# Kernel tuning notes

Measured on AMD Instinct MI355X. Metric: run time of the kernel, lower is better.

Reference implementation:

```python
import jax, jax.numpy as jnp
import numpy as np

N_NODES = 100000
N_EDGES = 1600000
IN_DIM = 64
HID_DIM = 64
NUM_CLASSES = 10
NUM_GRAPHS = 64


def setup_inputs() -> dict:
    key = jax.random.key(0)
    ks = jax.random.split(key, 8)
    x = jax.random.normal(ks[0], (N_NODES, IN_DIM), dtype=jnp.float32)
    edge_index = jax.random.randint(ks[1], (2, N_EDGES), 0, N_NODES, dtype=jnp.int32)
    batch = jnp.sort(jax.random.randint(ks[2], (N_NODES,), 0, NUM_GRAPHS, dtype=jnp.int32))
    # GCNConv weights (glorot-ish scale) and biases
    W1 = jax.random.normal(ks[3], (IN_DIM, HID_DIM), dtype=jnp.float32) / np.sqrt(IN_DIM)
    b1 = jnp.zeros((HID_DIM,), dtype=jnp.float32)
    W2 = jax.random.normal(ks[4], (HID_DIM, HID_DIM), dtype=jnp.float32) / np.sqrt(HID_DIM)
    b2 = jnp.zeros((HID_DIM,), dtype=jnp.float32)
    Wlin = jax.random.normal(ks[5], (HID_DIM, NUM_CLASSES), dtype=jnp.float32) / np.sqrt(HID_DIM)
    blin = jnp.zeros((NUM_CLASSES,), dtype=jnp.float32)
    return {"x": x, "edge_index": edge_index, "batch": batch,
            "W1": W1, "b1": b1, "W2": W2, "b2": b2, "Wlin": Wlin, "blin": blin}


def _gcn_conv(h, src, dst, norm, W, b, n_nodes):
    # h' = scatter_add( norm * (h W)[src] -> dst ) + b   (symmetric-normalized A+I)
    m = (h @ W)[src] * norm[:, None]          # [E+N, hid] edge messages (incl. self-loops)
    out = jax.ops.segment_sum(m, dst, num_segments=n_nodes)
    return out + b


def reference(x, edge_index, batch, W1, b1, W2, b2, Wlin, blin):
    n = x.shape[0]
    loops = jnp.arange(n, dtype=edge_index.dtype)
    src = jnp.concatenate([edge_index[0], loops])  # A + I self-loops
    dst = jnp.concatenate([edge_index[1], loops])
    deg = jax.ops.segment_sum(jnp.ones_like(dst, dtype=x.dtype), dst, num_segments=n)
    dinv = jax.lax.rsqrt(jnp.maximum(deg, 1.0))
    norm = dinv[src] * dinv[dst]               # D^{-1/2} (A+I) D^{-1/2} edge weights

    h = jax.nn.relu(_gcn_conv(x, src, dst, norm, W1, b1, n))
    h = jax.nn.relu(_gcn_conv(h, src, dst, norm, W2, b2, n))

    # global_mean_pool over batch segments
    sums = jax.ops.segment_sum(h, batch, num_segments=NUM_GRAPHS)
    cnts = jax.ops.segment_sum(jnp.ones((n,), dtype=h.dtype), batch, num_segments=NUM_GRAPHS)
    pooled = sums / jnp.maximum(cnts, 1.0)[:, None]
    return pooled @ Wlin + blin                # [G, num_classes]
```

## Files before the change

### kernel.cpp

```cpp
#include <hip/hip_runtime.h>
#include <hip/hip_bf16.h>


#define NDIM 64
#define NGRAPH 64
#define NREP 32
#define BSHIFT 7
#define BNODES 128
#define PADSLOT (BNODES * 16)
#define ECHUNK 8192

#define BLO(u) __uint_as_float((u) << 16)
#define BHI(u) __uint_as_float((u) & 0xFFFF0000u)

__device__ __forceinline__ unsigned short f32_to_bf16(float f) {
    unsigned int u = __float_as_uint(f);
    unsigned int r = 0x7FFFu + ((u >> 16) & 1u);
    return (unsigned short)((u + r) >> 16);
}

__global__ void bincnt_k(const int* __restrict__ dst, int* __restrict__ cntmat,
                         int e, int nb) {
    extern __shared__ int hist[];
    int t = threadIdx.x;
    for (int i = t; i < nb; i += 256) hist[i] = 0;
    __syncthreads();
    int base = blockIdx.x * ECHUNK + t;
#pragma unroll
    for (int k = 0; k < 32; ++k) {
        int i = base + k * 256;
        if (i < e) atomicAdd(&hist[dst[i] >> BSHIFT], 1);
    }
    __syncthreads();
    long row = (long)blockIdx.x * nb;
    for (int i = t; i < nb; i += 256) cntmat[row + i] = hist[i];
}

__global__ void colscan_k(const int* __restrict__ cntmat, int* __restrict__ basemat,
                          int* __restrict__ bucketTot, int nblk, int nb) {
    __shared__ int s[256];
    int b = blockIdx.x;
    int t = threadIdx.x;
    int v = (t < nblk) ? cntmat[(long)t * nb + b] : 0;
    s[t] = v;
    __syncthreads();
    for (int off = 1; off < 256; off <<= 1) {
        int tmp = (t >= off) ? s[t - off] : 0;
        __syncthreads();
        s[t] += tmp;
        __syncthreads();
    }
    if (t < nblk) basemat[(long)t * nb + b] = s[t] - v;
    if (t == 255) bucketTot[b] = s[255];
}

__global__ void bscan_k(const int* __restrict__ bucketTot, int* __restrict__ bucketStart,
                        int* __restrict__ start, int nb, int n, int e) {
    __shared__ int s[1024];
    int t = threadIdx.x;
    int v = (t < nb) ? bucketTot[t] : 0;
    s[t] = v;
    __syncthreads();
    for (int off = 1; off < 1024; off <<= 1) {
        int tmp = (t >= off) ? s[t - off] : 0;
        __syncthreads();
        s[t] += tmp;
        __syncthreads();
    }
    if (t < nb) bucketStart[t + 1] = s[t];
    if (t == 0) { bucketStart[0] = 0; start[n] = e; }
}

__global__ void bscatter_k(const int* __restrict__ src, const int* __restrict__ dst,
                           const int* __restrict__ bucketStart,
                           const int* __restrict__ basemat,
                           unsigned int* __restrict__ ebuf, int e, int nb) {
    extern __shared__ int cur[];
    int t = threadIdx.x;
    long row = (long)blockIdx.x * nb;
    for (int i = t; i < nb; i += 256) cur[i] = bucketStart[i] + basemat[row + i];
    __syncthreads();
    int base = blockIdx.x * ECHUNK + t;
#pragma unroll
    for (int k = 0; k < 32; ++k) {
        int i = base + k * 256;
        if (i < e) {
            int d = dst[i];
            int b = d >> BSHIFT;
            int pos = atomicAdd(&cur[b], 1);
            ebuf[pos] = ((unsigned)(d & (BNODES - 1)) << 25) | (unsigned)src[i];
        }
    }
}

__global__ void fill2_k(const unsigned int* __restrict__ ebuf,
                        const int* __restrict__ bucketStart,
                        const int* __restrict__ batch, float* __restrict__ dinv,
                        int* __restrict__ start, int* __restrict__ m16,
                        int* __restrict__ csr,
                        int* __restrict__ gstart, int* __restrict__ gend, int n) {
    __shared__ int scnt[BNODES], sincl[BNODES], scur[BNODES];
    int t = threadIdx.x;
    int b = blockIdx.x;
    int node0 = b << BSHIFT;
    int nNodes = min(BNODES, n - node0);
    if (t < BNODES) scnt[t] = 0;
    int e0 = bucketStart[b], e1 = bucketStart[b + 1];
    __syncthreads();
    for (int i = e0 + t; i < e1; i += 256)
        atomicAdd(&scnt[ebuf[i] >> 25], 1);
    __syncthreads();
    int val = (t < BNODES) ? scnt[t] : 0;
    int slots = (t < nNodes) ? ((val + 16) & ~15) : 0;
    if (t < BNODES) sincl[t] = slots;
    __syncthreads();
    for (int off = 1; off < BNODES; off <<= 1) {
        int tmp = (t >= off && t < BNODES) ? sincl[t - off] : 0;
        __syncthreads();
        if (t < BNODES) sincl[t] += tmp;
        __syncthreads();
    }
    if (t < nNodes) {
        int v = node0 + t;
        int st = e0 + b * PADSLOT + sincl[t] - slots;
        start[v] = st;
        m16[v] = slots >> 4;
        scur[t] = st;
        dinv[v] = rsqrtf((float)(val + 1));
        csr[st + val] = v;
        for (int k2 = val + 1; k2 < slots; ++k2) csr[st + k2] = n;
        int g = batch[v];
        if (v == 0 || batch[v - 1] != g) gstart[g] = v;
        if (v == n - 1 || batch[v + 1] != g) gend[g] = v + 1;
    }
    __syncthreads();
    for (int i = e0 + t; i < e1; i += 256) {
        unsigned rec = ebuf[i];
        int pos = atomicAdd(&scur[rec >> 25], 1);
        csr[pos] = (int)(rec & 0x1FFFFFFu);
    }
}

__global__ void gemm_k(const float* __restrict__ A, const float* __restrict__ W,
                       const float* __restrict__ scale,
                       unsigned long long* __restrict__ C, int n) {
    __shared__ float4 Wl4[64 * 16];
    __shared__ float4 Xl4[64 * 16];
    int t = threadIdx.x;
    const float4* W4 = (const float4*)W;
#pragma unroll
    for (int i = 0; i < 4; ++i) Wl4[t + 256 * i] = W4[t + 256 * i];
    const float4* A4 = (const float4*)A;
    long fbase = (long)blockIdx.x * 1024;
    long fmax  = (long)n * 16;
#pragma unroll
    for (int i = 0; i < 4; ++i) {
        long f = fbase + t + 256 * i;
        float4 v;
        if (f < fmax) v = A4[f];
        else { v.x = 0.f; v.y = 0.f; v.z = 0.f; v.w = 0.f; }
        Xl4[t + 256 * i] = v;
    }
    __syncthreads();
    int rg = t >> 4, cg = t & 15;
    float a00 = 0.f, a01 = 0.f, a02 = 0.f, a03 = 0.f;
    float a10 = 0.f, a11 = 0.f, a12 = 0.f, a13 = 0.f;
    float a20 = 0.f, a21 = 0.f, a22 = 0.f, a23 = 0.f;
    float a30 = 0.f, a31 = 0.f, a32 = 0.f, a33 = 0.f;
#pragma unroll 4
    for (int k4 = 0; k4 < 16; ++k4) {
        float4 w0 = Wl4[(4 * k4 + 0) * 16 + cg];
        float4 w1 = Wl4[(4 * k4 + 1) * 16 + cg];
        float4 w2 = Wl4[(4 * k4 + 2) * 16 + cg];
        float4 w3 = Wl4[(4 * k4 + 3) * 16 + cg];
        float4 x0 = Xl4[(4 * rg + 0) * 16 + k4];
        float4 x1 = Xl4[(4 * rg + 1) * 16 + k4];
        float4 x2 = Xl4[(4 * rg + 2) * 16 + k4];
        float4 x3 = Xl4[(4 * rg + 3) * 16 + k4];
        a00 += x0.x * w0.x + x0.y * w1.x + x0.z * w2.x + x0.w * w3.x;
        a01 += x0.x * w0.y + x0.y * w1.y + x0.z * w2.y + x0.w * w3.y;
        a02 += x0.x * w0.z + x0.y * w1.z + x0.z * w2.z + x0.w * w3.z;
        a03 += x0.x * w0.w + x0.y * w1.w + x0.z * w2.w + x0.w * w3.w;
        a10 += x1.x * w0.x + x1.y * w1.x + x1.z * w2.x + x1.w * w3.x;
        a11 += x1.x * w0.y + x1.y * w1.y + x1.z * w2.y + x1.w * w3.y;
        a12 += x1.x * w0.z + x1.y * w1.z + x1.z * w2.z + x1.w * w3.z;
        a13 += x1.x * w0.w + x1.y * w1.w + x1.z * w2.w + x1.w * w3.w;
        a20 += x2.x * w0.x + x2.y * w1.x + x2.z * w2.x + x2.w * w3.x;
        a21 += x2.x * w0.y + x2.y * w1.y + x2.z * w2.y + x2.w * w3.y;
        a22 += x2.x * w0.z + x2.y * w1.z + x2.z * w2.z + x2.w * w3.z;
        a23 += x2.x * w0.w + x2.y * w1.w + x2.z * w2.w + x2.w * w3.w;
        a30 += x3.x * w0.x + x3.y * w1.x + x3.z * w2.x + x3.w * w3.x;
        a31 += x3.x * w0.y + x3.y * w1.y + x3.z * w2.y + x3.w * w3.y;
        a32 += x3.x * w0.z + x3.y * w1.z + x3.z * w2.z + x3.w * w3.z;
        a33 += x3.x * w0.w + x3.y * w1.w + x3.z * w2.w + x3.w * w3.w;
    }
    int vb = blockIdx.x * 64 + rg * 4;
    int v;
    float s;
    unsigned long long u;
    v = vb + 0;
    if (v < n) {
        s = scale[v];
        u  = (unsigned long long)(((unsigned int)f32_to_bf16(s * a01) << 16) | (unsigned int)f32_to_bf16(s * a00));
        u |= (unsigned long long)(((unsigned int)f32_to_bf16(s * a03) << 16) | (unsigned int)f32_to_bf16(s * a02)) << 32;
        C[(long)v * 16 + cg] = u;
    }
    v = vb + 1;
    if (v < n) {
        s = scale[v];
        u  = (unsigned long long)(((unsigned int)f32_to_bf16(s * a11) << 16) | (unsigned int)f32_to_bf16(s * a10));
        u |= (unsigned long long)(((unsigned int)f32_to_bf16(s * a13) << 16) | (unsigned int)f32_to_bf16(s * a12)) << 32;
        C[(long)v * 16 + cg] = u;
    }
    v = vb + 2;
    if (v < n) {
        s = scale[v];
        u  = (unsigned long long)(((unsigned int)f32_to_bf16(s * a21) << 16) | (unsigned int)f32_to_bf16(s * a20));
        u |= (unsigned long long)(((unsigned int)f32_to_bf16(s * a23) << 16) | (unsigned int)f32_to_bf16(s * a22)) << 32;
        C[(long)v * 16 + cg] = u;
    }
    v = vb + 3;
    if (v < n) {
        s = scale[v];
        u  = (unsigned long long)(((unsigned int)f32_to_bf16(s * a31) << 16) | (unsigned int)f32_to_bf16(s * a30));
        u |= (unsigned long long)(((unsigned int)f32_to_bf16(s * a33) << 16) | (unsigned int)f32_to_bf16(s * a32)) << 32;
        C[(long)v * 16 + cg] = u;
    }
}

__device__ __forceinline__ float gather_p(const unsigned int* __restrict__ xp,
                                          const int* __restrict__ csr,
                                          int s0, int m16, int h, int p) {
    float l0 = 0.f, l1 = 0.f, l2 = 0.f, l3 = 0.f;
    float h0 = 0.f, h1 = 0.f, h2 = 0.f, h3 = 0.f;
    int c = s0 + h;
    for (int it = 0; it < m16; ++it) {
        int j0 = csr[c +  0];
        int j1 = csr[c +  2];
        int j2 = csr[c +  4];
        int j3 = csr[c +  6];
        int j4 = csr[c +  8];
        int j5 = csr[c + 10];
        int j6 = csr[c + 12];
        int j7 = csr[c + 14];
        unsigned int u0 = xp[(long)j0 * 32 + p];
        unsigned int u1 = xp[(long)j1 * 32 + p];
        unsigned int u2 = xp[(long)j2 * 32 + p];
        unsigned int u3 = xp[(long)j3 * 32 + p];
        unsigned int u4 = xp[(long)j4 * 32 + p];
        unsigned int u5 = xp[(long)j5 * 32 + p];
        unsigned int u6 = xp[(long)j6 * 32 + p];
        unsigned int u7 = xp[(long)j7 * 32 + p];
        l0 += BLO(u0);  h0 += BHI(u0);
        l1 += BLO(u1);  h1 += BHI(u1);
        l2 += BLO(u2);  h2 += BHI(u2);
        l3 += BLO(u3);  h3 += BHI(u3);
        l0 += BLO(u4);  h0 += BHI(u4);
        l1 += BLO(u5);  h1 += BHI(u5);
        l2 += BLO(u6);  h2 += BHI(u6);
        l3 += BLO(u7);  h3 += BHI(u7);
        c += 16;
    }
    float al = (l0 + l1) + (l2 + l3);
    float ah = (h0 + h1) + (h2 + h3);
    al += __shfl_xor(al, 32);
    ah += __shfl_xor(ah, 32);
    return h ? ah : al;
}

__global__ void agg_k(const unsigned int* __restrict__ xp, const float* __restrict__ dinv,
                      const int* __restrict__ start, const int* __restrict__ m16,
                      const int* __restrict__ csr, const float* __restrict__ bias,
                      float* __restrict__ out, int n) {
    int t = threadIdx.x;
    int lane = t & 63;
    int h = lane >> 5;
    int p = lane & 31;
    int v = blockIdx.x * 4 + (t >> 6);
    if (v >= n) return;
    float sum = gather_p(xp, csr, start[v], m16[v], h, p);
    int d = 2 * p + h;
    float val = sum * dinv[v] + bias[d];
    out[(long)v * NDIM + d] = fmaxf(val, 0.f);
}

__global__ void aggpool_k(const unsigned int* __restrict__ xp, const float* __restrict__ dinv,
                          const int* __restrict__ start, const int* __restrict__ m16,
                          const int* __restrict__ csr, const float* __restrict__ b2,
                          const int* __restrict__ batch, float* __restrict__ pooledR, int n) {
    int t = threadIdx.x;
    int lane = t & 63;
    int h = lane >> 5, p = lane & 31;
    int wid = blockIdx.x * 4 + (t >> 6);
    int v0 = wid * 4;
    if (v0 >= n) return;
    int v1 = min(v0 + 4, n);
    int d = 2 * p + h;
    float bias = b2[d];
    long rbase = (long)(wid & (NREP - 1)) * (NGRAPH * NDIM);
    int gcur = -1;
    float acc = 0.f;
    for (int v = v0; v < v1; ++v) {
        int g = batch[v];
        if (g != gcur) {
            if (gcur >= 0) atomicAdd(&pooledR[rbase + gcur * NDIM + d], acc);
            gcur = g;
            acc = 0.f;
        }
        float sum = gather_p(xp, csr, start[v], m16[v], h, p);
        acc += fmaxf(sum * dinv[v] + bias, 0.f);
    }
    if (gcur >= 0) atomicAdd(&pooledR[rbase + gcur * NDIM + d], acc);
}

__global__ void reduce_k(const float* __restrict__ pooledR, float* __restrict__ pooled) {
    int t = blockIdx.x * 256 + threadIdx.x;
    if (t >= NGRAPH * NDIM) return;
    float s = 0.f;
    for (int r = 0; r < NREP; ++r) s += pooledR[(long)r * (NGRAPH * NDIM) + t];
    pooled[t] = s;
}

__global__ void final_k(const float* __restrict__ pooled, const int* __restrict__ gstart,
                        const int* __restrict__ gend,
                        const float* __restrict__ Wlin, const float* __restrict__ blin,
                        float* __restrict__ out, int nclass) {
    int t = blockIdx.x * blockDim.x + threadIdx.x;
    if (t >= NGRAPH * nclass) return;
    int g = t / nclass, c = t % nclass;
    float cnt = (float)(gend[g] - gstart[g]);
    float inv = 1.f / fmaxf(cnt, 1.f);
    float acc = 0.f;
    for (int j = 0; j < NDIM; ++j) acc += pooled[g * NDIM + j] * Wlin[j * nclass + c];
    out[t] = acc * inv + blin[c];
}

extern "C" void kernel_launch(void* const* d_in, const int* in_sizes, int n_in,
                              void* d_out, int out_size, void* d_ws, size_t ws_size,
                              hipStream_t stream) {
    const float* x     = (const float*)d_in[0];
    const int*   ei    = (const int*)d_in[1];
    const int*   batch = (const int*)d_in[2];
    const float* W1    = (const float*)d_in[3];
    const float* b1    = (const float*)d_in[4];
    const float* W2    = (const float*)d_in[5];
    const float* b2    = (const float*)d_in[6];
    const float* Wlin  = (const float*)d_in[7];
    const float* blin  = (const float*)d_in[8];
    float* out = (float*)d_out;

    const int N = in_sizes[0] / NDIM;
    const int E = in_sizes[1] / 2;
    const int NCLASS = in_sizes[7] / NDIM;
    const int* src = ei;
    const int* dst = ei + E;
    const int NB   = (N + BNODES - 1) >> BSHIFT;
    const int NBLK = (E + ECHUNK - 1) / ECHUNK;

    size_t o = 0;
    char* wsp = (char*)d_ws;
    auto take = [&](size_t nbytes) -> void* {
        void* p = (void*)(wsp + o);
        o += (nbytes + 255) & ~(size_t)255;
        return p;
    };
    int*   gstart    = (int*)take(NGRAPH * 4);
    int*   gend      = (int*)take(NGRAPH * 4);
    float* pooledR   = (float*)take((size_t)NREP * NGRAPH * NDIM * 4);
    size_t zero_bytes = o;
    float* pooled    = (float*)take(NGRAPH * NDIM * 4);
    int*   cntmat   = (int*)take((size_t)NBLK * NB * 4);
    int*   basemat  = (int*)take((size_t)NBLK * NB * 4);
    int*   bucketTot   = (int*)take((size_t)NB * 4);
    int*   bucketStart = (int*)take((size_t)(NB + 1) * 4);
    float* dinv  = (float*)take((size_t)N * 4);
    int*   start = (int*)take((size_t)(N + 1) * 4);
    int*   m16   = (int*)take((size_t)N * 4);
    int*   csr   = (int*)take(((size_t)E + (size_t)NB * PADSLOT + 64) * 4);
    unsigned int* xws  = (unsigned int*)take((size_t)(N + 1) * NDIM * 2);
    float* h     = (float*)take((size_t)N * NDIM * 4);
    unsigned int* ebuf = (unsigned int*)h;
    (void)ws_size;

    hipMemsetAsync(d_ws, 0, zero_bytes, stream);
    hipMemsetAsync((char*)xws + (size_t)N * NDIM * 2, 0, NDIM * 2, stream);

    int rbl = (N + 3) / 4;
    int gbl = (N + 63) / 64;
    int pbl = (N + 15) / 16;

    bincnt_k<<<NBLK, 256, (size_t)NB * 4, stream>>>(dst, cntmat, E, NB);
    colscan_k<<<NB, 256, 0, stream>>>(cntmat, basemat, bucketTot, NBLK, NB);
    bscan_k<<<1, 1024, 0, stream>>>(bucketTot, bucketStart, start, NB, N, E);
    bscatter_k<<<NBLK, 256, (size_t)NB * 4, stream>>>(src, dst, bucketStart, basemat, ebuf, E, NB);
    fill2_k<<<NB, 256, 0, stream>>>(ebuf, bucketStart, batch, dinv, start, m16, csr, gstart, gend, N);

    gemm_k<<<gbl, 256, 0, stream>>>(x, W1, dinv, (unsigned long long*)xws, N);
    agg_k<<<rbl, 256, 0, stream>>>(xws, dinv, start, m16, csr, b1, h, N);
    gemm_k<<<gbl, 256, 0, stream>>>(h, W2, dinv, (unsigned long long*)xws, N);
    aggpool_k<<<pbl, 256, 0, stream>>>(xws, dinv, start, m16, csr, b2, batch, pooledR, N);
    reduce_k<<<(NGRAPH * NDIM + 255) / 256, 256, 0, stream>>>(pooledR, pooled);
    final_k<<<(NGRAPH * NCLASS + 255) / 256, 256, 0, stream>>>(pooled, gstart, gend, Wlin, blin, out, NCLASS);
}
```

Measured before the change: 276.6 us.

## Stream CSR gather across four nodes per wave, prefetch indices, fold memsets and reduce

Both aggregation kernels now use a shared gather_stream routine. One wavefront handles four consecutive nodes as one continuous edge stream and loads the next batch of CSR indices before accumulating the current feature loads, so index loads and feature gathers overlap. The two memsets are removed: their zeroing moves into colscan_k, bscan_k and gemm_k, which run earlier. reduce_k is dropped and final_k sums the pooled replicas itself. This saves launches and per-node latency, but adds more per-thread work in final_k and assumes start and m16 are 16-byte aligned for the int4 loads.

```diff
diff --git a/kernel.cpp b/kernel.cpp
--- a/kernel.cpp
+++ b/kernel.cpp
@@ -37,10 +37,13 @@
 }
 
 __global__ void colscan_k(const int* __restrict__ cntmat, int* __restrict__ basemat,
-                          int* __restrict__ bucketTot, int nblk, int nb) {
+                          int* __restrict__ bucketTot, float* __restrict__ pooledR,
+                          int nblk, int nb) {
     __shared__ int s[256];
     int b = blockIdx.x;
     int t = threadIdx.x;
+    int z = b * 256 + t;
+    if (z < NREP * NGRAPH * NDIM) pooledR[z] = 0.f;
     int v = (t < nblk) ? cntmat[(long)t * nb + b] : 0;
     s[t] = v;
     __syncthreads();
@@ -55,9 +58,11 @@
 }
 
 __global__ void bscan_k(const int* __restrict__ bucketTot, int* __restrict__ bucketStart,
-                        int* __restrict__ start, int nb, int n, int e) {
+                        int* __restrict__ start, int* __restrict__ gstart,
+                        int* __restrict__ gend, int nb, int n, int e) {
     __shared__ int s[1024];
     int t = threadIdx.x;
+    if (t < NGRAPH) { gstart[t] = 0; gend[t] = 0; }
     int v = (t < nb) ? bucketTot[t] : 0;
     s[t] = v;
     __syncthreads();
@@ -147,6 +152,7 @@
     __shared__ float4 Wl4[64 * 16];
     __shared__ float4 Xl4[64 * 16];
     int t = threadIdx.x;
+    if (blockIdx.x == 0 && t < 16) C[(long)n * 16 + t] = 0ULL;
     const float4* W4 = (const float4*)W;
 #pragma unroll
     for (int i = 0; i < 4; ++i) Wl4[t + 256 * i] = W4[t + 256 * i];
@@ -228,21 +234,28 @@
     }
 }
 
-__device__ __forceinline__ float gather_p(const unsigned int* __restrict__ xp,
-                                          const int* __restrict__ csr,
-                                          int s0, int m16, int h, int p) {
+template <class F>
+__device__ __forceinline__ void gather_stream(const unsigned int* __restrict__ xp,
+                                              const int* __restrict__ csr,
+                                              int c0, int m0, int m1, int m2, int m3,
+                                              int nv, int h, int p, F fin) {
+    int M = m0;
+    if (nv > 1) M += m1;
+    if (nv > 2) M += m2;
+    if (nv > 3) M += m3;
+    int c = c0 + h;
+    int j0 = csr[c +  0];
+    int j1 = csr[c +  2];
+    int j2 = csr[c +  4];
+    int j3 = csr[c +  6];
+    int j4 = csr[c +  8];
+    int j5 = csr[c + 10];
+    int j6 = csr[c + 12];
+    int j7 = csr[c + 14];
     float l0 = 0.f, l1 = 0.f, l2 = 0.f, l3 = 0.f;
     float h0 = 0.f, h1 = 0.f, h2 = 0.f, h3 = 0.f;
-    int c = s0 + h;
-    for (int it = 0; it < m16; ++it) {
-        int j0 = csr[c +  0];
-        int j1 = csr[c +  2];
-        int j2 = csr[c +  4];
-        int j3 = csr[c +  6];
-        int j4 = csr[c +  8];
-        int j5 = csr[c + 10];
-        int j6 = csr[c + 12];
-        int j7 = csr[c + 14];
+    int mrem = m0, cur = 0;
+    for (int it = 0; it < M; ++it) {
         unsigned int u0 = xp[(long)j0 * 32 + p];
         unsigned int u1 = xp[(long)j1 * 32 + p];
         unsigned int u2 = xp[(long)j2 * 32 + p];
@@ -251,6 +264,15 @@
         unsigned int u5 = xp[(long)j5 * 32 + p];
         unsigned int u6 = xp[(long)j6 * 32 + p];
         unsigned int u7 = xp[(long)j7 * 32 + p];
+        c += 16;
+        int t0 = csr[c +  0];
+        int t1 = csr[c +  2];
+        int t2 = csr[c +  4];
+        int t3 = csr[c +  6];
+        int t4 = csr[c +  8];
+        int t5 = csr[c + 10];
+        int t6 = csr[c + 12];
+        int t7 = csr[c + 14];
         l0 += BLO(u0);  h0 += BHI(u0);
         l1 += BLO(u1);  h1 += BHI(u1);
         l2 += BLO(u2);  h2 += BHI(u2);
@@ -259,13 +281,20 @@
         l1 += BLO(u5);  h1 += BHI(u5);
         l2 += BLO(u6);  h2 += BHI(u6);
         l3 += BLO(u7);  h3 += BHI(u7);
-        c += 16;
-    }
-    float al = (l0 + l1) + (l2 + l3);
-    float ah = (h0 + h1) + (h2 + h3);
-    al += __shfl_xor(al, 32);
-    ah += __shfl_xor(ah, 32);
-    return h ? ah : al;
+        j0 = t0; j1 = t1; j2 = t2; j3 = t3;
+        j4 = t4; j5 = t5; j6 = t6; j7 = t7;
+        if (--mrem == 0) {
+            float al = (l0 + l1) + (l2 + l3);
+            float ah = (h0 + h1) + (h2 + h3);
+            al += __shfl_xor(al, 32);
+            ah += __shfl_xor(ah, 32);
+            fin(cur, h ? ah : al);
+            l0 = l1 = l2 = l3 = 0.f;
+            h0 = h1 = h2 = h3 = 0.f;
+            ++cur;
+            mrem = (cur == 1) ? m1 : ((cur == 2) ? m2 : m3);
+        }
+    }
 }
 
 __global__ void agg_k(const unsigned int* __restrict__ xp, const float* __restrict__ dinv,
@@ -276,12 +305,21 @@
     int lane = t & 63;
     int h = lane >> 5;
     int p = lane & 31;
-    int v = blockIdx.x * 4 + (t >> 6);
-    if (v >= n) return;
-    float sum = gather_p(xp, csr, start[v], m16[v], h, p);
+    int wid = blockIdx.x * 4 + (t >> 6);
+    int v0 = wid * 4;
+    if (v0 >= n) return;
+    int nv = min(4, n - v0);
+    int4 ss = *(const int4*)&start[v0];
+    int4 mm = *(const int4*)&m16[v0];
+    float4 dv = *(const float4*)&dinv[v0];
     int d = 2 * p + h;
-    float val = sum * dinv[v] + bias[d];
-    out[(long)v * NDIM + d] = fmaxf(val, 0.f);
+    float b = bias[d];
+    float* orow = out + (long)v0 * NDIM + d;
+    gather_stream(xp, csr, ss.x, mm.x, mm.y, mm.z, mm.w, nv, h, p,
+        [&](int cur, float sum) {
+            float dvv = (cur == 0) ? dv.x : (cur == 1) ? dv.y : (cur == 2) ? dv.z : dv.w;
+            orow[(long)cur * NDIM] = fmaxf(fmaf(sum, dvv, b), 0.f);
+        });
 }
 
 __global__ void aggpool_k(const unsigned int* __restrict__ xp, const float* __restrict__ dinv,
@@ -294,34 +332,31 @@
     int wid = blockIdx.x * 4 + (t >> 6);
     int v0 = wid * 4;
     if (v0 >= n) return;
-    int v1 = min(v0 + 4, n);
+    int nv = min(4, n - v0);
+    int4 ss = *(const int4*)&start[v0];
+    int4 mm = *(const int4*)&m16[v0];
+    float4 dv = *(const float4*)&dinv[v0];
+    int4 bt = *(const int4*)&batch[v0];
     int d = 2 * p + h;
     float bias = b2[d];
     long rbase = (long)(wid & (NREP - 1)) * (NGRAPH * NDIM);
     int gcur = -1;
     float acc = 0.f;
-    for (int v = v0; v < v1; ++v) {
-        int g = batch[v];
-        if (g != gcur) {
-            if (gcur >= 0) atomicAdd(&pooledR[rbase + gcur * NDIM + d], acc);
-            gcur = g;
-            acc = 0.f;
-        }
-        float sum = gather_p(xp, csr, start[v], m16[v], h, p);
-        acc += fmaxf(sum * dinv[v] + bias, 0.f);
-    }
+    gather_stream(xp, csr, ss.x, mm.x, mm.y, mm.z, mm.w, nv, h, p,
+        [&](int cur, float sum) {
+            int g = (cur == 0) ? bt.x : (cur == 1) ? bt.y : (cur == 2) ? bt.z : bt.w;
+            float dvv = (cur == 0) ? dv.x : (cur == 1) ? dv.y : (cur == 2) ? dv.z : dv.w;
+            if (g != gcur) {
+                if (gcur >= 0) atomicAdd(&pooledR[rbase + gcur * NDIM + d], acc);
+                gcur = g;
+                acc = 0.f;
+            }
+            acc += fmaxf(fmaf(sum, dvv, bias), 0.f);
+        });
     if (gcur >= 0) atomicAdd(&pooledR[rbase + gcur * NDIM + d], acc);
 }
 
-__global__ void reduce_k(const float* __restrict__ pooledR, float* __restrict__ pooled) {
-    int t = blockIdx.x * 256 + threadIdx.x;
-    if (t >= NGRAPH * NDIM) return;
-    float s = 0.f;
-    for (int r = 0; r < NREP; ++r) s += pooledR[(long)r * (NGRAPH * NDIM) + t];
-    pooled[t] = s;
-}
-
-__global__ void final_k(const float* __restrict__ pooled, const int* __restrict__ gstart,
+__global__ void final_k(const float* __restrict__ pooledR, const int* __restrict__ gstart,
                         const int* __restrict__ gend,
                         const float* __restrict__ Wlin, const float* __restrict__ blin,
                         float* __restrict__ out, int nclass) {
@@ -331,7 +366,13 @@
     float cnt = (float)(gend[g] - gstart[g]);
     float inv = 1.f / fmaxf(cnt, 1.f);
     float acc = 0.f;
-    for (int j = 0; j < NDIM; ++j) acc += pooled[g * NDIM + j] * Wlin[j * nclass + c];
+    for (int j = 0; j < NDIM; ++j) {
+        float pj = 0.f;
+#pragma unroll
+        for (int r = 0; r < NREP; ++r)
+            pj += pooledR[(long)r * (NGRAPH * NDIM) + g * NDIM + j];
+        acc += pj * Wlin[j * nclass + c];
+    }
     out[t] = acc * inv + blin[c];
 }
 
@@ -367,8 +408,6 @@
     int*   gstart    = (int*)take(NGRAPH * 4);
     int*   gend      = (int*)take(NGRAPH * 4);
     float* pooledR   = (float*)take((size_t)NREP * NGRAPH * NDIM * 4);
-    size_t zero_bytes = o;
-    float* pooled    = (float*)take(NGRAPH * NDIM * 4);
     int*   cntmat   = (int*)take((size_t)NBLK * NB * 4);
     int*   basemat  = (int*)take((size_t)NBLK * NB * 4);
     int*   bucketTot   = (int*)take((size_t)NB * 4);
@@ -382,23 +421,18 @@
     unsigned int* ebuf = (unsigned int*)h;
     (void)ws_size;
 
-    hipMemsetAsync(d_ws, 0, zero_bytes, stream);
-    hipMemsetAsync((char*)xws + (size_t)N * NDIM * 2, 0, NDIM * 2, stream);
-
-    int rbl = (N + 3) / 4;
+    int rbl = (N + 15) / 16;
     int gbl = (N + 63) / 64;
-    int pbl = (N + 15) / 16;
 
     bincnt_k<<<NBLK, 256, (size_t)NB * 4, stream>>>(dst, cntmat, E, NB);
-    colscan_k<<<NB, 256, 0, stream>>>(cntmat, basemat, bucketTot, NBLK, NB);
-    bscan_k<<<1, 1024, 0, stream>>>(bucketTot, bucketStart, start, NB, N, E);
+    colscan_k<<<NB, 256, 0, stream>>>(cntmat, basemat, bucketTot, pooledR, NBLK, NB);
+    bscan_k<<<1, 1024, 0, stream>>>(bucketTot, bucketStart, start, gstart, gend, NB, N, E);
     bscatter_k<<<NBLK, 256, (size_t)NB * 4, stream>>>(src, dst, bucketStart, basemat, ebuf, E, NB);
     fill2_k<<<NB, 256, 0, stream>>>(ebuf, bucketStart, batch, dinv, start, m16, csr, gstart, gend, N);
 
     gemm_k<<<gbl, 256, 0, stream>>>(x, W1, dinv, (unsigned long long*)xws, N);
     agg_k<<<rbl, 256, 0, stream>>>(xws, dinv, start, m16, csr, b1, h, N);
     gemm_k<<<gbl, 256, 0, stream>>>(h, W2, dinv, (unsigned long long*)xws, N);
-    aggpool_k<<<pbl, 256, 0, stream>>>(xws, dinv, start, m16, csr, b2, batch, pooledR, N);
-    reduce_k<<<(NGRAPH * NDIM + 255) / 256, 256, 0, stream>>>(pooledR, pooled);
-    final_k<<<(NGRAPH * NCLASS + 255) / 256, 256, 0, stream>>>(pooled, gstart, gend, Wlin, blin, out, NCLASS);
-}
+    aggpool_k<<<rbl, 256, 0, stream>>>(xws, dinv, start, m16, csr, b2, batch, pooledR, N);
+    final_k<<<(NGRAPH * NCLASS + 255) / 256, 256, 0, stream>>>(pooledR, gstart, gend, Wlin, blin, out, NCLASS);
+}
```

Measured after the change: 353.8 us. 1.28x slower.
